# Optimization experiments

Hardware: AMD Instinct MI355X
Metric: run time of the kernel (lower is better)

The kernel has to match this reference:

```python
import jax, jax.numpy as jnp
import numpy as np

N, E, D, L = 100000, 1_600_000, 128, 8


def setup_inputs() -> dict:
    key = jax.random.key(0)
    k0, k1, k2 = jax.random.split(key, 3)
    x = jax.random.normal(k0, (N, D), dtype=jnp.float32)
    edge_index = jax.random.randint(k1, (2, E), 0, N, dtype=jnp.int64)
    Ws = jax.random.normal(k2, (L, D, D), dtype=jnp.float32) / np.float32(np.sqrt(D))
    bs = jnp.zeros((L, D), dtype=jnp.float32)
    return {"x": x, "edge_index": edge_index, "Ws": Ws, "bs": bs}


def _gcn_conv(h, W, b, src, dst, norm_edge, self_norm):
    """PyG GCNConv: linear -> sym-normalized aggregate (with self loops) -> +bias."""
    h = h @ W                                    # [N, D]
    msg = h[src] * norm_edge[:, None]            # [E, D] gather + scale
    agg = jax.ops.segment_sum(msg, dst, num_segments=h.shape[0])  # scatter-add
    return agg + h * self_norm[:, None] + b      # self-loop term fused in


def reference(x, edge_index, Ws, bs):
    src, dst = edge_index[0], edge_index[1]
    # degree of (A + I) on target nodes, symmetric normalization
    deg = jax.ops.segment_sum(jnp.ones((src.shape[0],), jnp.float32), dst,
                              num_segments=x.shape[0]) + 1.0
    dis = deg ** -0.5                            # deg >= 1, safe
    norm_edge = dis[src] * dis[dst]              # per-edge norm
    self_norm = dis * dis                        # per-node self-loop norm

    n_layers = Ws.shape[0]
    h = x
    initial = x
    for i in range(n_layers):
        h = _gcn_conv(h, Ws[i], bs[i], src, dst, norm_edge, self_norm)
        if i > 0:
            h = h + initial
            initial = h
        h = jax.nn.relu(h)
        if i < n_layers - 1:
            # NOTE: at i == 0 the original indexes layers[-1] (last layer) — faithful.
            j = i - 1
            h = h + _gcn_conv(h, Ws[j], bs[j], src, dst, norm_edge, self_norm)
    return h
```

## Files before the change

### kernel.cpp

```cpp
#include <hip/hip_runtime.h>

#define D 128
#define SCAN_CH 1024
#define SA_STRIDE 136
#define SC_STRIDE 132
#define NPB 64
#define CONV_THREADS 512

typedef _Float16 f16x8 __attribute__((ext_vector_type(8)));
typedef float f32x4 __attribute__((ext_vector_type(4)));


__global__ void hist_kernel(const int* __restrict__ dst, int* __restrict__ counts,
                            int E, int N) {
  int range = blockIdx.x & 7;
  int lo = (int)(((long long)N * range) >> 3);
  int hi = (int)(((long long)N * (range + 1)) >> 3);
  int stride = (gridDim.x >> 3) * blockDim.x;
  for (int e = (blockIdx.x >> 3) * blockDim.x + threadIdx.x; e < E; e += stride) {
    int d = dst[e];
    if (d >= lo && d < hi) atomicAdd(&counts[d], 1);
  }
}

__global__ void fill_kernel(const int* __restrict__ src, const int* __restrict__ dst,
    int* __restrict__ fillp, int* __restrict__ csr_src, int E, int N) {
  int range = blockIdx.x & 7;
  int lo = (int)(((long long)N * range) >> 3);
  int hi = (int)(((long long)N * (range + 1)) >> 3);
  int stride = (gridDim.x >> 3) * blockDim.x;
  for (int e = (blockIdx.x >> 3) * blockDim.x + threadIdx.x; e < E; e += stride) {
    int d = dst[e];
    if (d >= lo && d < hi) {
      int s = src[e];
      int p = atomicAdd(&fillp[d], 1);
      csr_src[p] = s;
    }
  }
}

__global__ void dis_kernel(const int* __restrict__ counts, float2* __restrict__ dnr, int N) {
  int n = blockIdx.x * blockDim.x + threadIdx.x;
  if (n < N) {
    float c = (float)counts[n] + 1.0f;
    dnr[n] = make_float2(rsqrtf(c), sqrtf(c));
  }
}

__global__ __launch_bounds__(256) void scan_phaseA(const int* __restrict__ counts,
    int* __restrict__ blksum, int N) {
  __shared__ int red[256];
  int base = blockIdx.x * SCAN_CH;
  int t = threadIdx.x;
  int s = 0;
  #pragma unroll
  for (int j = 0; j < 4; ++j) {
    int idx = base + t * 4 + j;
    if (idx < N) s += counts[idx];
  }
  red[t] = s;
  __syncthreads();
  for (int d = 128; d > 0; d >>= 1) {
    if (t < d) red[t] += red[t + d];
    __syncthreads();
  }
  if (t == 0) blksum[blockIdx.x] = red[0];
}

__global__ __launch_bounds__(1024) void scan_phaseB(int* __restrict__ blksum, int NB) {
  __shared__ int sa[1024], sb[1024];
  int t = threadIdx.x;
  int v = (t < NB) ? blksum[t] : 0;
  sa[t] = v;
  __syncthreads();
  int* a = sa; int* b = sb;
  for (int d = 1; d < 1024; d <<= 1) {
    int val = a[t] + ((t >= d) ? a[t - d] : 0);
    b[t] = val;
    __syncthreads();
    int* tmp = a; a = b; b = tmp;
  }
  if (t < NB) blksum[t] = a[t] - v;
}

__global__ __launch_bounds__(256) void scan_phaseC(const int* __restrict__ counts,
    const int* __restrict__ blksum, int* __restrict__ row_ptr, int* __restrict__ fillp, int N) {
  __shared__ int ra[256], rb[256];
  int base = blockIdx.x * SCAN_CH;
  int t = threadIdx.x;
  int v[4]; int s = 0;
  #pragma unroll
  for (int j = 0; j < 4; ++j) {
    int idx = base + t * 4 + j;
    v[j] = (idx < N) ? counts[idx] : 0;
    s += v[j];
  }
  ra[t] = s;
  __syncthreads();
  int* a = ra; int* b = rb;
  for (int d = 1; d < 256; d <<= 1) {
    int val = a[t] + ((t >= d) ? a[t - d] : 0);
    b[t] = val;
    __syncthreads();
    int* tmp = a; a = b; b = tmp;
  }
  int excl = a[t] - s + blksum[blockIdx.x];
  #pragma unroll
  for (int j = 0; j < 4; ++j) {
    int idx = base + t * 4 + j;
    if (idx < N) {
      row_ptr[idx] = excl;
      fillp[idx] = excl;
      excl += v[j];
      if (idx == N - 1) row_ptr[N] = excl;
    }
  }
}


__global__ void conv_x_kernel(const float* __restrict__ x, const float2* __restrict__ dnr,
    _Float16* __restrict__ hs, int total8) {
  int i = blockIdx.x * blockDim.x + threadIdx.x;
  if (i >= total8) return;
  int node = i >> 4;
  float dn = dnr[node].x;
  const float4* p = (const float4*)(x + (size_t)i * 8);
  float4 a = p[0], b = p[1];
  f16x8 v;
  v[0] = (_Float16)(dn * a.x); v[1] = (_Float16)(dn * a.y);
  v[2] = (_Float16)(dn * a.z); v[3] = (_Float16)(dn * a.w);
  v[4] = (_Float16)(dn * b.x); v[5] = (_Float16)(dn * b.y);
  v[6] = (_Float16)(dn * b.z); v[7] = (_Float16)(dn * b.w);
  *(f16x8*)(hs + (size_t)i * 8) = v;
}

__global__ void repack_w_kernel(const float* __restrict__ Ws, _Float16* __restrict__ Wf, int total) {
  int t = blockIdx.x * blockDim.x + threadIdx.x;
  if (t >= total) return;
  int lane = t & 63;
  int nb = (t >> 6) & 7;
  int kb = (t >> 9) & 3;
  int l = t >> 11;
  int col = nb * 16 + (lane & 15);
  int k0 = kb * 32 + (lane >> 4) * 8;
  const float* w = Ws + (size_t)l * D * D;
  f16x8 v;
  #pragma unroll
  for (int j = 0; j < 8; ++j) v[j] = (_Float16)w[(k0 + j) * D + col];
  *(f16x8*)(Wf + (size_t)t * 8) = v;
}

__global__ __launch_bounds__(CONV_THREADS) void conv_fused_kernel(
    const _Float16* __restrict__ hs, const int* __restrict__ row_ptr,
    const int* __restrict__ csr_src, const float2* __restrict__ dnr,
    const f16x8* __restrict__ Wf, const float* __restrict__ bias,
    const float* __restrict__ init_in, float* __restrict__ init_out,
    float* __restrict__ out, _Float16* __restrict__ hs_out, int N, int flags) {
  __shared__ __align__(16) char smem[NPB * SC_STRIDE * 4];
  _Float16* sA = (_Float16*)smem;
  float* sC = (float*)smem;
  int tid = threadIdx.x;
  int node0 = blockIdx.x * NPB;
  int ng = tid >> 4;
  int li = tid & 15;
  int c0 = li * 8;

  float2 dr[2];
  f16x8 ownr[2];

  #pragma unroll
  for (int k = 0; k < 2; ++k) {
    int lr = ng + 32 * k;
    int n = node0 + lr;
    f16x8 g = {};
    if (n < N) {
      float acc[8];
      #pragma unroll
      for (int j = 0; j < 8; ++j) acc[j] = 0.f;
      int beg = row_ptr[n], end = row_ptr[n + 1];
      #pragma unroll 4
      for (int e = beg; e < end; ++e) {
        int s = csr_src[e];
        f16x8 v = *(const f16x8*)&hs[(size_t)s * D + c0];
        #pragma unroll
        for (int j = 0; j < 8; ++j) acc[j] += (float)v[j];
      }
      f16x8 own = *(const f16x8*)&hs[(size_t)n * D + c0];
      float2 d2 = dnr[n];
      dr[k] = d2;
      ownr[k] = own;
      #pragma unroll
      for (int j = 0; j < 8; ++j) g[j] = (_Float16)(d2.x * (acc[j] + (float)own[j]));
    }
    *(f16x8*)&sA[lr * SA_STRIDE + c0] = g;
  }

  int wave = tid >> 6, lane = tid & 63;
  f16x8 bf[4];
  #pragma unroll
  for (int kb = 0; kb < 4; ++kb)
    bf[kb] = Wf[(kb * 8 + wave) * 64 + lane];
  __syncthreads();

  f32x4 ca[4];
  #pragma unroll
  for (int rt = 0; rt < 4; ++rt) ca[rt] = (f32x4){0, 0, 0, 0};
  #pragma unroll
  for (int rt = 0; rt < 4; ++rt) {
    #pragma unroll
    for (int kb = 0; kb < 4; ++kb) {
      f16x8 a = *(const f16x8*)&sA[(rt * 16 + (lane & 15)) * SA_STRIDE + kb * 32 + (lane >> 4) * 8];
      ca[rt] = __builtin_amdgcn_mfma_f32_16x16x32_f16(a, bf[kb], ca[rt], 0, 0, 0);
    }
  }
  __syncthreads();

  {
    int colb = wave * 16 + (lane & 15);
    int rowb = (lane >> 4) * 4;
    #pragma unroll
    for (int rt = 0; rt < 4; ++rt)
      #pragma unroll
      for (int r = 0; r < 4; ++r)
        sC[(rt * 16 + rowb + r) * SC_STRIDE + colb] = ca[rt][r];
  }
  __syncthreads();

  float4 b0 = *(const float4*)&bias[c0];
  float4 b1 = *(const float4*)&bias[c0 + 4];
  #pragma unroll
  for (int k = 0; k < 2; ++k) {
    int lr = ng + 32 * k;
    int n = node0 + lr;
    if (n >= N) continue;
    float v[8];
    float4 s0 = *(const float4*)&sC[lr * SC_STRIDE + c0];
    float4 s1 = *(const float4*)&sC[lr * SC_STRIDE + c0 + 4];
    v[0] = s0.x + b0.x; v[1] = s0.y + b0.y; v[2] = s0.z + b0.z; v[3] = s0.w + b0.w;
    v[4] = s1.x + b1.x; v[5] = s1.y + b1.y; v[6] = s1.z + b1.z; v[7] = s1.w + b1.w;
    size_t off = (size_t)n * D + c0;
    if (flags & 8) {
      float rd = dr[k].y;
      #pragma unroll
      for (int j = 0; j < 8; ++j) v[j] += (float)ownr[k][j] * rd;
    }
    if (flags & 1) {
      float4 i0 = *(const float4*)&init_in[off];
      float4 i1 = *(const float4*)&init_in[off + 4];
      v[0] += i0.x; v[1] += i0.y; v[2] += i0.z; v[3] += i0.w;
      v[4] += i1.x; v[5] += i1.y; v[6] += i1.z; v[7] += i1.w;
    }
    if (flags & 2) {
      *(float4*)&init_out[off]     = make_float4(v[0], v[1], v[2], v[3]);
      *(float4*)&init_out[off + 4] = make_float4(v[4], v[5], v[6], v[7]);
    }
    if (flags & 4) {
      #pragma unroll
      for (int j = 0; j < 8; ++j) v[j] = fmaxf(v[j], 0.f);
    }
    if (flags & 32) {
      *(float4*)&out[off]     = make_float4(v[0], v[1], v[2], v[3]);
      *(float4*)&out[off + 4] = make_float4(v[4], v[5], v[6], v[7]);
    }
    if (flags & 16) {
      float dn = dr[k].x;
      f16x8 h8;
      #pragma unroll
      for (int j = 0; j < 8; ++j) h8[j] = (_Float16)(dn * v[j]);
      *(f16x8*)&hs_out[off] = h8;
    }
  }
}


extern "C" void kernel_launch(void* const* d_in, const int* in_sizes, int n_in,
                              void* d_out, int out_size, void* d_ws, size_t ws_size,
                              hipStream_t stream) {
  const float* x = (const float*)d_in[0];
  const int* ei = (const int*)d_in[1];
  const float* Ws = (const float*)d_in[2];
  const float* bs = (const float*)d_in[3];
  float* out = (float*)d_out;

  const int N = in_sizes[0] / D;
  const int E = in_sizes[1] / 2;
  const int L = in_sizes[2] / (D * D);
  const int* src = ei;
  const int* dst = ei + E;

  uintptr_t p = (uintptr_t)d_ws;
  auto alloc = [&](size_t bytes) {
    uintptr_t r = p;
    p = (r + bytes + 255) & ~(uintptr_t)255;
    return r;
  };
  float2*    dnr      = (float2*)alloc((size_t)N * 8);
  int*       counts   = (int*)  alloc((size_t)N * 4);
  int*       row_ptr  = (int*)  alloc((size_t)(N + 1) * 4);
  int*       fillp    = (int*)  alloc((size_t)N * 4);
  int*       blksum   = (int*)  alloc((size_t)1024 * 4);
  int*       csr_src  = (int*)  alloc((size_t)E * 4);
  _Float16*  hs_a     = (_Float16*)alloc((size_t)N * D * 2);
  _Float16*  hs_b     = (_Float16*)alloc((size_t)N * D * 2);
  float*     init_buf = (float*)alloc((size_t)N * D * 4);
  _Float16*  Wf       = (_Float16*)alloc((size_t)L * 4 * 8 * 64 * 8 * 2);

  const int NB = (N + SCAN_CH - 1) / SCAN_CH;

  hipMemsetAsync(counts, 0, (size_t)N * 4, stream);
  hist_kernel<<<8 * 192, 256, 0, stream>>>(dst, counts, E, N);
  dis_kernel<<<(N + 255) / 256, 256, 0, stream>>>(counts, dnr, N);
  scan_phaseA<<<NB, 256, 0, stream>>>(counts, blksum, N);
  scan_phaseB<<<1, 1024, 0, stream>>>(blksum, NB);
  scan_phaseC<<<NB, 256, 0, stream>>>(counts, blksum, row_ptr, fillp, N);
  fill_kernel<<<8 * 192, 256, 0, stream>>>(src, dst, fillp, csr_src, E, N);
  conv_x_kernel<<<(N * 16 + 255) / 256, 256, 0, stream>>>(x, dnr, hs_a, N * 16);
  {
    int total = L * 2048;
    repack_w_kernel<<<(total + 255) / 256, 256, 0, stream>>>(Ws, Wf, total);
  }

  const int conv_grid = (N + NPB - 1) / NPB;
  _Float16* hsp[2] = {hs_a, hs_b};
  int cur = 0;

  for (int i = 0; i < L; ++i) {
    int flags;
    if (i == 0)          flags = 4 | 16;
    else if (i == L - 1) flags = 1 | 4 | 32;
    else                 flags = 1 | 2 | 4 | 16;
    const float* init_in = (i <= 1) ? x : (const float*)init_buf;
    conv_fused_kernel<<<conv_grid, CONV_THREADS, 0, stream>>>(hsp[cur], row_ptr, csr_src, dnr,
        (const f16x8*)(Wf + (size_t)i * 2048 * 8), bs + (size_t)i * D,
        init_in, init_buf, out, hsp[cur ^ 1], N, flags);
    if (flags & 16) cur ^= 1;
    if (i < L - 1) {
      int j = (i == 0) ? (L - 1) : (i - 1);
      conv_fused_kernel<<<conv_grid, CONV_THREADS, 0, stream>>>(hsp[cur], row_ptr, csr_src, dnr,
          (const f16x8*)(Wf + (size_t)j * 2048 * 8), bs + (size_t)j * D,
          nullptr, nullptr, out, hsp[cur ^ 1], N, 8 | 16);
      cur ^= 1;
    }
  }
}
```

Baseline: 1.290 ms.

## Degree-sort nodes, narrow gather lanes, unroll edge loop, store residual in fp16

Adds a counting sort of nodes by in-degree (descending, capped at 255) and makes the fused conv kernel process nodes in that permuted order, so blocks see similar degrees and load imbalance drops. Each node is now handled by 32 lanes of 4 halfs instead of 16 lanes of 8, and the edge loop is unrolled by 8 so more independent gathers are in flight. The residual buffer between layers changes from fp32 to fp16, halving its read and write traffic. The costs are three extra setup kernels, scattered output writes because of the permutation, and lower precision in the residual path.

Result: slower. 1.896 ms (+47.0%).

```diff
diff --git a/kernel.cpp b/kernel.cpp
--- a/kernel.cpp
+++ b/kernel.cpp
@@ -8,6 +8,7 @@
 #define CONV_THREADS 512
 
 typedef _Float16 f16x8 __attribute__((ext_vector_type(8)));
+typedef _Float16 f16x4 __attribute__((ext_vector_type(4)));
 typedef float f32x4 __attribute__((ext_vector_type(4)));
 
 
@@ -114,6 +115,48 @@
       excl += v[j];
       if (idx == N - 1) row_ptr[N] = excl;
     }
+  }
+}
+
+
+__global__ __launch_bounds__(256) void keyhist_kernel(const int* __restrict__ counts,
+    int* __restrict__ ghist, int N) {
+  __shared__ int lh[256];
+  int t = threadIdx.x;
+  lh[t] = 0;
+  __syncthreads();
+  for (int n = blockIdx.x * 256 + t; n < N; n += gridDim.x * 256) {
+    int k = 255 - min(counts[n], 255);
+    atomicAdd(&lh[k], 1);
+  }
+  __syncthreads();
+  if (lh[t]) atomicAdd(&ghist[t], lh[t]);
+}
+
+__global__ __launch_bounds__(256) void keyscan_kernel(const int* __restrict__ ghist,
+    int* __restrict__ binwork) {
+  __shared__ int a_[256], b_[256];
+  int t = threadIdx.x;
+  int v = ghist[t];
+  a_[t] = v;
+  __syncthreads();
+  int* a = a_; int* b = b_;
+  for (int d = 1; d < 256; d <<= 1) {
+    int val = a[t] + ((t >= d) ? a[t - d] : 0);
+    b[t] = val;
+    __syncthreads();
+    int* tmp = a; a = b; b = tmp;
+  }
+  binwork[t] = a[t] - v;
+}
+
+__global__ void scatter_perm_kernel(const int* __restrict__ counts,
+    int* __restrict__ binwork, int* __restrict__ perm, int N) {
+  int n = blockIdx.x * blockDim.x + threadIdx.x;
+  if (n < N) {
+    int k = 255 - min(counts[n], 255);
+    int p = atomicAdd(&binwork[k], 1);
+    perm[p] = n;
   }
 }
 
@@ -153,46 +196,71 @@
 __global__ __launch_bounds__(CONV_THREADS) void conv_fused_kernel(
     const _Float16* __restrict__ hs, const int* __restrict__ row_ptr,
     const int* __restrict__ csr_src, const float2* __restrict__ dnr,
-    const f16x8* __restrict__ Wf, const float* __restrict__ bias,
-    const float* __restrict__ init_in, float* __restrict__ init_out,
+    const int* __restrict__ perm, const f16x8* __restrict__ Wf,
+    const float* __restrict__ bias, const float* __restrict__ init32,
+    const _Float16* __restrict__ init16in, _Float16* __restrict__ init16out,
     float* __restrict__ out, _Float16* __restrict__ hs_out, int N, int flags) {
   __shared__ __align__(16) char smem[NPB * SC_STRIDE * 4];
   _Float16* sA = (_Float16*)smem;
   float* sC = (float*)smem;
   int tid = threadIdx.x;
   int node0 = blockIdx.x * NPB;
-  int ng = tid >> 4;
-  int li = tid & 15;
-  int c0 = li * 8;
-
-  float2 dr[2];
-  f16x8 ownr[2];
-
-  #pragma unroll
-  for (int k = 0; k < 2; ++k) {
-    int lr = ng + 32 * k;
-    int n = node0 + lr;
-    f16x8 g = {};
-    if (n < N) {
-      float acc[8];
-      #pragma unroll
-      for (int j = 0; j < 8; ++j) acc[j] = 0.f;
+  int g32 = tid >> 5;
+  int li = tid & 31;
+  int c0 = li * 4;
+
+  int nsv[4];
+  float2 dr[4];
+  f16x4 ownr[4];
+
+  #pragma unroll
+  for (int k = 0; k < 4; ++k) {
+    int lr = g32 + 16 * k;
+    int idx = node0 + lr;
+    int n = (idx < N) ? perm[idx] : -1;
+    nsv[k] = n;
+    f16x4 g = {};
+    if (n >= 0) {
+      float a0 = 0.f, a1 = 0.f, a2 = 0.f, a3 = 0.f;
       int beg = row_ptr[n], end = row_ptr[n + 1];
-      #pragma unroll 4
-      for (int e = beg; e < end; ++e) {
+      int e = beg;
+      for (; e + 8 <= end; e += 8) {
+        int s0 = csr_src[e + 0], s1 = csr_src[e + 1];
+        int s2 = csr_src[e + 2], s3 = csr_src[e + 3];
+        int s4 = csr_src[e + 4], s5 = csr_src[e + 5];
+        int s6 = csr_src[e + 6], s7 = csr_src[e + 7];
+        f16x4 v0 = *(const f16x4*)&hs[(size_t)s0 * D + c0];
+        f16x4 v1 = *(const f16x4*)&hs[(size_t)s1 * D + c0];
+        f16x4 v2 = *(const f16x4*)&hs[(size_t)s2 * D + c0];
+        f16x4 v3 = *(const f16x4*)&hs[(size_t)s3 * D + c0];
+        f16x4 v4 = *(const f16x4*)&hs[(size_t)s4 * D + c0];
+        f16x4 v5 = *(const f16x4*)&hs[(size_t)s5 * D + c0];
+        f16x4 v6 = *(const f16x4*)&hs[(size_t)s6 * D + c0];
+        f16x4 v7 = *(const f16x4*)&hs[(size_t)s7 * D + c0];
+        a0 += (float)v0[0] + (float)v1[0] + (float)v2[0] + (float)v3[0]
+            + (float)v4[0] + (float)v5[0] + (float)v6[0] + (float)v7[0];
+        a1 += (float)v0[1] + (float)v1[1] + (float)v2[1] + (float)v3[1]
+            + (float)v4[1] + (float)v5[1] + (float)v6[1] + (float)v7[1];
+        a2 += (float)v0[2] + (float)v1[2] + (float)v2[2] + (float)v3[2]
+            + (float)v4[2] + (float)v5[2] + (float)v6[2] + (float)v7[2];
+        a3 += (float)v0[3] + (float)v1[3] + (float)v2[3] + (float)v3[3]
+            + (float)v4[3] + (float)v5[3] + (float)v6[3] + (float)v7[3];
+      }
+      for (; e < end; ++e) {
         int s = csr_src[e];
-        f16x8 v = *(const f16x8*)&hs[(size_t)s * D + c0];
-        #pragma unroll
-        for (int j = 0; j < 8; ++j) acc[j] += (float)v[j];
+        f16x4 v = *(const f16x4*)&hs[(size_t)s * D + c0];
+        a0 += (float)v[0]; a1 += (float)v[1]; a2 += (float)v[2]; a3 += (float)v[3];
       }
-      f16x8 own = *(const f16x8*)&hs[(size_t)n * D + c0];
+      f16x4 own = *(const f16x4*)&hs[(size_t)n * D + c0];
       float2 d2 = dnr[n];
       dr[k] = d2;
       ownr[k] = own;
-      #pragma unroll
-      for (int j = 0; j < 8; ++j) g[j] = (_Float16)(d2.x * (acc[j] + (float)own[j]));
-    }
-    *(f16x8*)&sA[lr * SA_STRIDE + c0] = g;
+      g[0] = (_Float16)(d2.x * (a0 + (float)own[0]));
+      g[1] = (_Float16)(d2.x * (a1 + (float)own[1]));
+      g[2] = (_Float16)(d2.x * (a2 + (float)own[2]));
+      g[3] = (_Float16)(d2.x * (a3 + (float)own[3]));
+    }
+    *(f16x4*)&sA[lr * SA_STRIDE + c0] = g;
   }
 
   int wave = tid >> 6, lane = tid & 63;
@@ -226,48 +294,46 @@
   }
   __syncthreads();
 
-  float4 b0 = *(const float4*)&bias[c0];
-  float4 b1 = *(const float4*)&bias[c0 + 4];
-  #pragma unroll
-  for (int k = 0; k < 2; ++k) {
-    int lr = ng + 32 * k;
-    int n = node0 + lr;
-    if (n >= N) continue;
-    float v[8];
+  float4 bv = *(const float4*)&bias[c0];
+  #pragma unroll
+  for (int k = 0; k < 4; ++k) {
+    int n = nsv[k];
+    if (n < 0) continue;
+    int lr = g32 + 16 * k;
     float4 s0 = *(const float4*)&sC[lr * SC_STRIDE + c0];
-    float4 s1 = *(const float4*)&sC[lr * SC_STRIDE + c0 + 4];
-    v[0] = s0.x + b0.x; v[1] = s0.y + b0.y; v[2] = s0.z + b0.z; v[3] = s0.w + b0.w;
-    v[4] = s1.x + b1.x; v[5] = s1.y + b1.y; v[6] = s1.z + b1.z; v[7] = s1.w + b1.w;
+    float v0 = s0.x + bv.x, v1 = s0.y + bv.y, v2 = s0.z + bv.z, v3 = s0.w + bv.w;
     size_t off = (size_t)n * D + c0;
     if (flags & 8) {
       float rd = dr[k].y;
-      #pragma unroll
-      for (int j = 0; j < 8; ++j) v[j] += (float)ownr[k][j] * rd;
+      v0 += (float)ownr[k][0] * rd; v1 += (float)ownr[k][1] * rd;
+      v2 += (float)ownr[k][2] * rd; v3 += (float)ownr[k][3] * rd;
     }
     if (flags & 1) {
-      float4 i0 = *(const float4*)&init_in[off];
-      float4 i1 = *(const float4*)&init_in[off + 4];
-      v[0] += i0.x; v[1] += i0.y; v[2] += i0.z; v[3] += i0.w;
-      v[4] += i1.x; v[5] += i1.y; v[6] += i1.z; v[7] += i1.w;
+      if (flags & 64) {
+        float4 iv = *(const float4*)&init32[off];
+        v0 += iv.x; v1 += iv.y; v2 += iv.z; v3 += iv.w;
+      } else {
+        f16x4 iv = *(const f16x4*)&init16in[off];
+        v0 += (float)iv[0]; v1 += (float)iv[1]; v2 += (float)iv[2]; v3 += (float)iv[3];
+      }
     }
     if (flags & 2) {
-      *(float4*)&init_out[off]     = make_float4(v[0], v[1], v[2], v[3]);
-      *(float4*)&init_out[off + 4] = make_float4(v[4], v[5], v[6], v[7]);
+      f16x4 o;
+      o[0] = (_Float16)v0; o[1] = (_Float16)v1; o[2] = (_Float16)v2; o[3] = (_Float16)v3;
+      *(f16x4*)&init16out[off] = o;
     }
     if (flags & 4) {
-      #pragma unroll
-      for (int j = 0; j < 8; ++j) v[j] = fmaxf(v[j], 0.f);
+      v0 = fmaxf(v0, 0.f); v1 = fmaxf(v1, 0.f); v2 = fmaxf(v2, 0.f); v3 = fmaxf(v3, 0.f);
     }
     if (flags & 32) {
-      *(float4*)&out[off]     = make_float4(v[0], v[1], v[2], v[3]);
-      *(float4*)&out[off + 4] = make_float4(v[4], v[5], v[6], v[7]);
+      *(float4*)&out[off] = make_float4(v0, v1, v2, v3);
     }
     if (flags & 16) {
       float dn = dr[k].x;
-      f16x8 h8;
-      #pragma unroll
-      for (int j = 0; j < 8; ++j) h8[j] = (_Float16)(dn * v[j]);
-      *(f16x8*)&hs_out[off] = h8;
+      f16x4 h;
+      h[0] = (_Float16)(dn * v0); h[1] = (_Float16)(dn * v1);
+      h[2] = (_Float16)(dn * v2); h[3] = (_Float16)(dn * v3);
+      *(f16x4*)&hs_out[off] = h;
     }
   }
 }
@@ -299,21 +365,28 @@
   int*       row_ptr  = (int*)  alloc((size_t)(N + 1) * 4);
   int*       fillp    = (int*)  alloc((size_t)N * 4);
   int*       blksum   = (int*)  alloc((size_t)1024 * 4);
+  int*       ghist    = (int*)  alloc((size_t)256 * 4);
+  int*       binwork  = (int*)  alloc((size_t)256 * 4);
+  int*       perm     = (int*)  alloc((size_t)N * 4);
   int*       csr_src  = (int*)  alloc((size_t)E * 4);
   _Float16*  hs_a     = (_Float16*)alloc((size_t)N * D * 2);
   _Float16*  hs_b     = (_Float16*)alloc((size_t)N * D * 2);
-  float*     init_buf = (float*)alloc((size_t)N * D * 4);
+  _Float16*  init16   = (_Float16*)alloc((size_t)N * D * 2);
   _Float16*  Wf       = (_Float16*)alloc((size_t)L * 4 * 8 * 64 * 8 * 2);
 
   const int NB = (N + SCAN_CH - 1) / SCAN_CH;
 
   hipMemsetAsync(counts, 0, (size_t)N * 4, stream);
+  hipMemsetAsync(ghist, 0, 256 * 4, stream);
   hist_kernel<<<8 * 192, 256, 0, stream>>>(dst, counts, E, N);
   dis_kernel<<<(N + 255) / 256, 256, 0, stream>>>(counts, dnr, N);
   scan_phaseA<<<NB, 256, 0, stream>>>(counts, blksum, N);
   scan_phaseB<<<1, 1024, 0, stream>>>(blksum, NB);
   scan_phaseC<<<NB, 256, 0, stream>>>(counts, blksum, row_ptr, fillp, N);
   fill_kernel<<<8 * 192, 256, 0, stream>>>(src, dst, fillp, csr_src, E, N);
+  keyhist_kernel<<<128, 256, 0, stream>>>(counts, ghist, N);
+  keyscan_kernel<<<1, 256, 0, stream>>>(ghist, binwork);
+  scatter_perm_kernel<<<(N + 255) / 256, 256, 0, stream>>>(counts, binwork, perm, N);
   conv_x_kernel<<<(N * 16 + 255) / 256, 256, 0, stream>>>(x, dnr, hs_a, N * 16);
   {
     int total = L * 2048;
@@ -329,16 +402,16 @@
     if (i == 0)          flags = 4 | 16;
     else if (i == L - 1) flags = 1 | 4 | 32;
     else                 flags = 1 | 2 | 4 | 16;
-    const float* init_in = (i <= 1) ? x : (const float*)init_buf;
-    conv_fused_kernel<<<conv_grid, CONV_THREADS, 0, stream>>>(hsp[cur], row_ptr, csr_src, dnr,
-        (const f16x8*)(Wf + (size_t)i * 2048 * 8), bs + (size_t)i * D,
-        init_in, init_buf, out, hsp[cur ^ 1], N, flags);
+    if (i == 1)          flags |= 64;
+    conv_fused_kernel<<<conv_grid, CONV_THREADS, 0, stream>>>(hsp[cur], row_ptr, csr_src,
+        dnr, perm, (const f16x8*)(Wf + (size_t)i * 2048 * 8), bs + (size_t)i * D,
+        x, init16, init16, out, hsp[cur ^ 1], N, flags);
     if (flags & 16) cur ^= 1;
     if (i < L - 1) {
       int j = (i == 0) ? (L - 1) : (i - 1);
-      conv_fused_kernel<<<conv_grid, CONV_THREADS, 0, stream>>>(hsp[cur], row_ptr, csr_src, dnr,
-          (const f16x8*)(Wf + (size_t)j * 2048 * 8), bs + (size_t)j * D,
-          nullptr, nullptr, out, hsp[cur ^ 1], N, 8 | 16);
+      conv_fused_kernel<<<conv_grid, CONV_THREADS, 0, stream>>>(hsp[cur], row_ptr, csr_src,
+          dnr, perm, (const f16x8*)(Wf + (size_t)j * 2048 * 8), bs + (size_t)j * D,
+          x, init16, init16, out, hsp[cur ^ 1], N, 8 | 16);
       cur ^= 1;
     }
   }
```
